# Kernel tuning notes

Hardware: AMD Instinct MI355X
Metric: run time of the kernel (lower is better)

## Reference

```python
import jax, jax.numpy as jnp
import numpy as np

B, N, I, O, CG, H, E = 32, 256, 16, 16, 64, 64, 4096
SEQ_LEN = 256  # sequence_length init arg (temporal attention scale)


def setup_inputs() -> dict:
    key = jax.random.key(0)
    ks = jax.random.split(key, 24)
    r = lambda i, shape, s: jax.random.normal(ks[i], shape, jnp.float32) * s
    return {
        'data': jax.random.normal(ks[0], (B, I, N), jnp.float32),
        'masks': jax.random.bernoulli(ks[1], 0.8, (B, I, N)),
        'edge_index': jax.random.randint(ks[2], (2, E), 0, N, jnp.int64),
        'gcn_w': r(3, (I, CG), 0.2),
        'gcn_b': jnp.zeros((CG,), jnp.float32),
        'sa_qw': r(4, (CG, CG), 0.1), 'sa_qb': jnp.zeros((CG,), jnp.float32),
        'sa_kw': r(5, (CG, CG), 0.1), 'sa_kb': jnp.zeros((CG,), jnp.float32),
        'gru_wih': r(6, (3 * H, I), 0.1), 'gru_whh': r(7, (3 * H, H), 0.1),
        'gru_bih': jnp.zeros((3 * H,), jnp.float32), 'gru_bhh': jnp.zeros((3 * H,), jnp.float32),
        'ta_qw': r(8, (H, H), 0.1), 'ta_qb': jnp.zeros((H,), jnp.float32),
        'ta_kw': r(9, (H, H), 0.1), 'ta_kb': jnp.zeros((H,), jnp.float32),
        'fc1_w': r(10, (H * N * 2, H * N // 4), 0.005), 'fc1_b': jnp.zeros((H * N // 4,), jnp.float32),
        'fc2_w': r(11, (H * N // 4, O * N), 0.01), 'fc2_b': jnp.zeros((O * N,), jnp.float32),
    }


def _forward(data, masks, edge_index, gcn_w, gcn_b, sa_qw, sa_qb, sa_kw, sa_kb,
             gru_wih, gru_whh, gru_bih, gru_bhh, ta_qw, ta_qb, ta_kw, ta_kb,
             fc1_w, fc1_b, fc2_w, fc2_b):
    data = jnp.where(masks, data, 0.0)            # [B, I, N]
    x = jnp.swapaxes(data, 1, 2)                  # [B, N, I] (per-sample node features)

    loop = jnp.arange(N)
    src = jnp.concatenate([edge_index[0], loop])
    dst = jnp.concatenate([edge_index[1], loop])
    w = jnp.concatenate([jnp.ones((E,), jnp.float32), 2.0 * jnp.ones((N,), jnp.float32)])
    deg = jax.ops.segment_sum(w, dst, num_segments=N)
    dinv = jnp.where(deg > 0, jax.lax.rsqrt(deg), 0.0)
    norm = dinv[src] * w * dinv[dst]              # [E+N]
    xw = x @ gcn_w                                # [B, N, CG]
    msg = xw[:, src, :] * norm[None, :, None]     # gather + scale
    agg = jax.vmap(lambda m: jax.ops.segment_sum(m, dst, num_segments=N))(msg)
    h = jax.nn.relu(agg + gcn_b)                  # [B, N, CG]

    # --- SpatialAttention (per sample, scale 1/sqrt(num_nodes)) ---
    q = h @ sa_qw + sa_qb
    k = h @ sa_kw + sa_kb
    att = jax.nn.softmax(jnp.einsum('bnc,bmc->bnm', q, k) / np.sqrt(N).astype(np.float32), axis=-1)
    ha = jnp.einsum('bnm,bmc->bnc', att, h)

    # torch stacks x.T -> [B, CG, N] then .view(B, -1, CG): a reshape, not a transpose
    se = jnp.swapaxes(h, 1, 2).reshape(B, N, CG)
    sa = jnp.swapaxes(ha, 1, 2).reshape(B, N, CG)
    # dropout is identity in eval mode

    # --- GRU (1 layer, batch_first) over rnn_input = data.view(B, -1, I) ---
    rnn_in = data.reshape(B, N, I)
    def step(hprev, xt):
        gi = xt @ gru_wih.T + gru_bih
        gh = hprev @ gru_whh.T + gru_bhh
        ir, iz, inn = jnp.split(gi, 3, axis=-1)
        hr, hz, hn = jnp.split(gh, 3, axis=-1)
        r = jax.nn.sigmoid(ir + hr)
        z = jax.nn.sigmoid(iz + hz)
        n = jnp.tanh(inn + r * hn)
        hnew = (1.0 - z) * n + z * hprev
        return hnew, hnew
    h0 = jnp.zeros((B, H), jnp.float32)
    _, outs = jax.lax.scan(step, h0, jnp.swapaxes(rnn_in, 0, 1))
    rnn_out = jnp.swapaxes(outs, 0, 1)            # [B, N, H]

    # --- TemporalAttention (scale 1/sqrt(sequence_length)) ---
    qt = rnn_out @ ta_qw + ta_qb
    kt = rnn_out @ ta_kw + ta_kb
    att_t = jax.nn.softmax(jnp.einsum('btc,bsc->bts', qt, kt) / np.sqrt(SEQ_LEN).astype(np.float32), axis=-1)
    rnn_a = jnp.einsum('bts,bsc->btc', att_t, rnn_out)

    # --- fused MLP combine ---
    embed = jnp.concatenate([rnn_out, se], axis=-1).reshape(B, -1)  # [B, 2*H*N]
    inter = embed @ fc1_w + fc1_b
    final = inter @ fc2_w + fc2_b
    final = jnp.swapaxes(final.reshape(B, N, O), 1, 2)              # [B, O, N]
    rnn_a = jnp.swapaxes(rnn_a, 1, 2)                               # [B, H, N]
    return final, sa, rnn_a


def reference(data, masks, edge_index, gcn_w, gcn_b, sa_qw, sa_qb, sa_kw, sa_kb,
              gru_wih, gru_whh, gru_bih, gru_bhh, ta_qw, ta_qb, ta_kw, ta_kb,
              fc1_w, fc1_b, fc2_w, fc2_b):
    return _forward(data, masks, edge_index, gcn_w, gcn_b, sa_qw, sa_qb, sa_kw, sa_kb,
                    gru_wih, gru_whh, gru_bih, gru_bhh, ta_qw, ta_qb, ta_kw, ta_kb,
                    fc1_w, fc1_b, fc2_w, fc2_b)
```

## Files before the change

kernel.cpp:

```cpp
#include <hip/hip_runtime.h>

#define NB 32
#define NN 256
#define NI 16
#define NO 16
#define NC 64
#define NH 64
#define NE 4096
#define FC1_N 4096

__device__ __forceinline__ float sigmoidf_(float x){ return 1.0f/(1.0f+__expf(-x)); }
__device__ __forceinline__ float tanhf_(float x){
  float e = __expf(2.0f*x);
  return 1.0f - 2.0f/(e+1.0f);
}

__global__ void k_detect(const unsigned char* __restrict__ m8, const int* __restrict__ ei, int* flags){
  int t = blockIdx.x*256 + threadIdx.x;
  unsigned a = (unsigned)m8[t*4+1] | (unsigned)m8[t*4+2] | (unsigned)m8[t*4+3];
  if (__any(a != 0) && (threadIdx.x & 63) == 0) atomicOr(&flags[0], 1);
  unsigned b = 0;
  if (t < 4096) b = (unsigned)ei[2*t+1];
  if (__any(b != 0) && (threadIdx.x & 63) == 0) atomicOr(&flags[1], 1);
}

__global__ void k_mask(const float* __restrict__ data, const unsigned char* __restrict__ m8,
                       const int* __restrict__ flags, float* __restrict__ dm){
  int i = blockIdx.x*256 + threadIdx.x;
  int mv = flags[0] ? (int)m8[i] : ((const int*)m8)[i];
  dm[i] = mv ? data[i] : 0.0f;
}

__device__ __forceinline__ int edge_src(const int* ei, const int* flags, int e){
  return flags[1] ? ei[e] : ei[2*e];
}
__device__ __forceinline__ int edge_dst(const int* ei, const int* flags, int e){
  return flags[1] ? ei[NE + e] : ei[2*(NE + e)];
}

__global__ __launch_bounds__(256) void k_graph(const int* __restrict__ ei, const int* __restrict__ flags,
                                               float* wadj){
  int t = threadIdx.x;
  float4 z = {0.f,0.f,0.f,0.f};
  for (int x = t; x < 16384; x += 256) ((float4*)wadj)[x] = z;
  __shared__ float degs[NN];
  __shared__ float dls[NN];
  degs[t] = 0.f;
  __syncthreads();
  for (int e = t; e < NE; e += 256) atomicAdd(&degs[edge_dst(ei, flags, e)], 1.0f);
  __syncthreads();
  float di = rsqrtf(degs[t] + 2.0f);
  dls[t] = di;
  atomicAdd(&wadj[t*NN + t], 2.0f*di*di);
  __syncthreads();
  for (int e = t; e < NE; e += 256){
    int s = edge_src(ei, flags, e), d = edge_dst(ei, flags, e);
    atomicAdd(&wadj[d*NN + s], dls[s]*dls[d]);
  }
}

__global__ void k_xw(const float* __restrict__ dm, const float* __restrict__ gw, float* __restrict__ xw){
  int idx = blockIdx.x*256 + threadIdx.x;
  int c = idx & 63, n = (idx>>6) & 255, b = idx>>14;
  const float* dmb = dm + b*NI*NN;
  float a = 0.f;
  #pragma unroll
  for (int i=0;i<NI;i++) a += dmb[i*NN + n]*gw[i*NC + c];
  xw[idx] = a;
}

__global__ void k_agg(const float* __restrict__ wadj, const float* __restrict__ xw,
                      const float* __restrict__ gb, float* __restrict__ h){
  int idx = blockIdx.x*256 + threadIdx.x;
  int c = idx & 63, n = (idx>>6) & 255, b = idx>>14;
  const float* wr = wadj + n*NN;
  const float* xb = xw + b*NN*NC + c;
  float a = gb[c];
  #pragma unroll 4
  for (int m=0;m<NN;m++) a += wr[m]*xb[m*NC];
  h[idx] = fmaxf(a, 0.0f);
}

__global__ void k_qk2(const float* __restrict__ hb, const float* __restrict__ rnn,
    const float* __restrict__ saqw, const float* __restrict__ saqb,
    const float* __restrict__ sakw, const float* __restrict__ sakb,
    const float* __restrict__ taqw, const float* __restrict__ taqb,
    const float* __restrict__ takw, const float* __restrict__ takb,
    float* __restrict__ qb, float* __restrict__ kb, float* __restrict__ qt, float* __restrict__ kt){
  int bid = blockIdx.x;
  const float *src, *qw, *qbias, *kw, *kbias; float *qo, *ko;
  if (bid < 2048){ src=hb; qw=saqw; qbias=saqb; kw=sakw; kbias=sakb; qo=qb; ko=kb; }
  else { bid -= 2048; src=rnn; qw=taqw; qbias=taqb; kw=takw; kbias=takb; qo=qt; ko=kt; }
  int idx = bid*256 + threadIdx.x;
  int c = idx & 63;
  const float* hr = src + (idx>>6)*NC;
  float aq = qbias[c], ak = kbias[c];
  #pragma unroll 8
  for (int cc=0; cc<NC; cc++){ float hv = hr[cc]; aq += hv*qw[cc*NC + c]; ak += hv*kw[cc*NC + c]; }
  qo[idx] = aq; ko[idx] = ak;
}

__global__ __launch_bounds__(256) void k_attn2(const float* __restrict__ qb, const float* __restrict__ kb,
    const float* __restrict__ hb, const float* __restrict__ qt, const float* __restrict__ kt,
    const float* __restrict__ rnn, float* __restrict__ out_sa, float* __restrict__ out_ra){
  int bidx = blockIdx.x;
  const float *q, *kmat, *v; float* outp;
  if (bidx < 1024){ q=qb; kmat=kb; v=hb; outp=out_sa; }
  else { bidx -= 1024; q=qt; kmat=kt; v=rnn; outp=out_ra; }
  int b = bidx >> 5, n0 = (bidx & 31)*8;
  int t = threadIdx.x;
  const float scale = 0.0625f;
  __shared__ __align__(16) float qs[8][64];
  __shared__ float S[8][256];
  #pragma unroll
  for (int rep=0; rep<2; rep++){
    int j = rep*256 + t; int r = j>>6, c = j&63;
    qs[r][c] = q[((b<<8) + n0 + r)*NC + c];
  }
  __syncthreads();
  float4 kr[16];
  const float4* kp = (const float4*)(kmat + ((b<<8) + t)*NC);
  #pragma unroll
  for (int i=0;i<16;i++) kr[i] = kp[i];
  #pragma unroll
  for (int r=0;r<8;r++){
    const float4* q4 = (const float4*)qs[r];
    float s = 0.f;
    #pragma unroll
    for (int i=0;i<16;i++){ float4 a=q4[i], bb=kr[i]; s += a.x*bb.x + a.y*bb.y + a.z*bb.z + a.w*bb.w; }
    S[r][t] = s*scale;
  }
  __syncthreads();
  {
    int g = t>>5, l = t&31;
    float vals[8];
    #pragma unroll
    for (int k2=0;k2<8;k2++) vals[k2] = S[g][l + (k2<<5)];
    float mx = vals[0];
    #pragma unroll
    for (int k2=1;k2<8;k2++) mx = fmaxf(mx, vals[k2]);
    #pragma unroll
    for (int off=16; off; off>>=1) mx = fmaxf(mx, __shfl_xor(mx, off));
    float sm = 0.f;
    #pragma unroll
    for (int k2=0;k2<8;k2++){ vals[k2] = __expf(vals[k2]-mx); sm += vals[k2]; }
    #pragma unroll
    for (int off=16; off; off>>=1) sm += __shfl_xor(sm, off);
    float rS = 1.0f/sm;
    #pragma unroll
    for (int k2=0;k2<8;k2++) S[g][l + (k2<<5)] = vals[k2]*rS;
  }
  __syncthreads();
  int c = t & 63, rp = t >> 6;
  const float* vp = v + (b<<8)*NC + c;
  float a0 = 0.f, a1 = 0.f;
  #pragma unroll 4
  for (int m=0;m<NN;m++){
    float vv = vp[m*NC];
    a0 += S[rp][m]*vv;
    a1 += S[rp+4][m]*vv;
  }
  outp[(((b<<6)+c)<<8) + n0 + rp]     = a0;
  outp[(((b<<6)+c)<<8) + n0 + rp + 4] = a1;
}

__global__ __launch_bounds__(192) void k_gru(const float* __restrict__ dm,
        const float* __restrict__ wih, const float* __restrict__ bih,
        const float* __restrict__ whh, const float* __restrict__ bhh,
        float* __restrict__ rnn){
  int b = blockIdx.x, j = threadIdx.x;
  __shared__ __align__(16) float dmS[4096];
  __shared__ __align__(16) float hs[64];
  __shared__ float gh[192];
  __shared__ float gin[64];
  float wh[64];
  const float4* wr = (const float4*)(whh + j*NH);
  #pragma unroll
  for (int k4=0;k4<16;k4++){ float4 t4 = wr[k4]; wh[4*k4]=t4.x; wh[4*k4+1]=t4.y; wh[4*k4+2]=t4.z; wh[4*k4+3]=t4.w; }
  float wi[16];
  const float4* wir = (const float4*)(wih + j*NI);
  #pragma unroll
  for (int k4=0;k4<4;k4++){ float4 t4 = wir[k4]; wi[4*k4]=t4.x; wi[4*k4+1]=t4.y; wi[4*k4+2]=t4.z; wi[4*k4+3]=t4.w; }
  float bj = bhh[j], bij = bih[j];
  const float4* dmb4 = (const float4*)(dm + b*4096);
  for (int x = j; x < 1024; x += 192) ((float4*)dmS)[x] = dmb4[x];
  if (j < 64) hs[j] = 0.f;
  __syncthreads();
  for (int t=0;t<NN;t++){
    const float* xt = &dmS[t*16];
    float gival = bij;
    #pragma unroll
    for (int i=0;i<16;i++) gival += wi[i]*xt[i];
    float a0=0.f,a1=0.f,a2=0.f,a3=0.f;
    #pragma unroll
    for (int k4=0;k4<16;k4++){
      float4 hv = *(const float4*)&hs[4*k4];
      a0 += wh[4*k4+0]*hv.x; a1 += wh[4*k4+1]*hv.y; a2 += wh[4*k4+2]*hv.z; a3 += wh[4*k4+3]*hv.w;
    }
    float ghv = a0+a1+a2+a3+bj;
    if (j < 128) gh[j] = ghv + gival;
    else { gh[j] = ghv; gin[j-128] = gival; }
    __syncthreads();
    if (j < 64){
      float r  = sigmoidf_(gh[j]);
      float z  = sigmoidf_(gh[j+64]);
      float nn = tanhf_   (gin[j] + r*gh[j+128]);
      float hn = nn + z*(hs[j]-nn);
      rnn[(b*NN + t)*NH + j] = hn;
      hs[j] = hn;
    }
    __syncthreads();
  }
}

__global__ void k_embedT(const float* __restrict__ rnn, const float* __restrict__ h,
                         float* __restrict__ ET){
  int idx = blockIdx.x*256 + threadIdx.x;
  int bb = idx & 31, rr = idx >> 5;
  int n = rr >> 7, c = rr & 127;
  float v;
  if (c < 64) v = rnn[((bb<<8) + n)*NH + c];
  else { int f = (n<<6) + (c-64); v = h[(bb<<14) + ((f&255)<<6) + (f>>8)]; }
  ET[idx] = v;
}

#define FMAQ(q, ev) { \
  acc[0][4*q+0]+=wv.x*ev.x; acc[1][4*q+0]+=wv.y*ev.x; acc[2][4*q+0]+=wv.z*ev.x; acc[3][4*q+0]+=wv.w*ev.x; \
  acc[0][4*q+1]+=wv.x*ev.y; acc[1][4*q+1]+=wv.y*ev.y; acc[2][4*q+1]+=wv.z*ev.y; acc[3][4*q+1]+=wv.w*ev.y; \
  acc[0][4*q+2]+=wv.x*ev.z; acc[1][4*q+2]+=wv.y*ev.z; acc[2][4*q+2]+=wv.z*ev.z; acc[3][4*q+2]+=wv.w*ev.z; \
  acc[0][4*q+3]+=wv.x*ev.w; acc[1][4*q+3]+=wv.y*ev.w; acc[2][4*q+3]+=wv.z*ev.w; acc[3][4*q+3]+=wv.w*ev.w; }

__global__ __launch_bounds__(512, 4) void k_fc1(const float* __restrict__ W,
                       const float* __restrict__ ET, float* __restrict__ part){
  const int tid = threadIdx.x, lane = tid & 63, w = tid >> 6;
  const int cw = w & 3, bh = w >> 2;
  const int col = blockIdx.x*1024 + cw*256 + lane*4;
  const int i0 = blockIdx.y*256;
  __shared__ __align__(16) float es[8][128*16];
  float4* esw4 = (float4*)es[w];
  float acc[4][16];
  #pragma unroll
  for (int c=0;c<4;c++)
    #pragma unroll
    for (int bb=0;bb<16;bb++) acc[c][bb]=0.f;
  const float* wp = W + (long)i0*FC1_N + col;
  float4 ring[4];
  #pragma unroll
  for (int p=0;p<4;p++) ring[p] = *(const float4*)(wp + (long)p*FC1_N);
  const float4* ET4 = (const float4*)ET;
  for (int c=0;c<2;c++){
    __syncthreads();
    const int rowbase = i0 + c*128;
    #pragma unroll
    for (int k=0;k<8;k++){
      int j = lane + k*64;
      esw4[j] = ET4[(long)(rowbase + (j>>2))*8 + bh*4 + (j&3)];
    }
    for (int ii4=0; ii4<32; ii4++){
      #pragma unroll
      for (int p=0;p<4;p++){
        const int r = c*128 + ii4*4 + p;
        float4 wv = ring[p];
        int pf = r + 4; pf = (pf < 256) ? pf : 255;
        ring[p] = *(const float4*)(wp + (long)pf*FC1_N);
        const int ib = (ii4*4 + p)*4;
        float4 e0 = esw4[ib+0], e1 = esw4[ib+1], e2 = esw4[ib+2], e3 = esw4[ib+3];
        FMAQ(0, e0) FMAQ(1, e1) FMAQ(2, e2) FMAQ(3, e3)
      }
    }
  }
  float* pp = part + (long)blockIdx.y*131072 + (long)(bh*16)*FC1_N + col;
  #pragma unroll
  for (int bb=0;bb<16;bb++){
    float4 o; o.x=acc[0][bb]; o.y=acc[1][bb]; o.z=acc[2][bb]; o.w=acc[3][bb];
    *(float4*)(pp + (long)bb*FC1_N) = o;
  }
}

__global__ void k_red1(const float* __restrict__ part, const float* __restrict__ bias,
                       float* __restrict__ ITr){
  int idx = blockIdx.x*256 + threadIdx.x;
  int b = idx >> 12, col = idx & 4095;
  float a = bias[col];
  #pragma unroll 16
  for (int y=0;y<128;y++) a += part[(long)y*131072 + b*FC1_N + col];
  ITr[col*32 + b] = a;
}

__global__ __launch_bounds__(256, 4) void k_fc2(const float* __restrict__ W,
                       const float* __restrict__ ITr, float* __restrict__ part){
  const int tid = threadIdx.x, lane = tid & 63, bq = tid >> 6;
  const int col = blockIdx.x*256 + lane*4;
  const int i0 = blockIdx.y*64;
  __shared__ __align__(16) float es[4][64*8];
  float4* esw4 = (float4*)es[bq];
  float acc[4][8];
  #pragma unroll
  for (int c=0;c<4;c++)
    #pragma unroll
    for (int bb=0;bb<8;bb++) acc[c][bb]=0.f;
  const float4* IT4 = (const float4*)ITr;
  #pragma unroll
  for (int k=0;k<2;k++){
    int j = lane + k*64;
    esw4[j] = IT4[(i0 + (j>>1))*8 + bq*2 + (j&1)];
  }
  const float* wp = W + (long)i0*FC1_N + col;
  float4 ring[4];
  #pragma unroll
  for (int p=0;p<4;p++) ring[p] = *(const float4*)(wp + (long)p*FC1_N);
  for (int ii4=0; ii4<16; ii4++){
    #pragma unroll
    for (int p=0;p<4;p++){
      const int r = ii4*4 + p;
      float4 wv = ring[p];
      int pf = r + 4; pf = (pf < 64) ? pf : 63;
      ring[p] = *(const float4*)(wp + (long)pf*FC1_N);
      float4 e0 = esw4[r*2+0], e1 = esw4[r*2+1];
      FMAQ(0, e0) FMAQ(1, e1)
    }
  }
  float* pp = part + (long)blockIdx.y*131072 + (long)(bq*8)*FC1_N + col;
  #pragma unroll
  for (int bb=0;bb<8;bb++){
    float4 o; o.x=acc[0][bb]; o.y=acc[1][bb]; o.z=acc[2][bb]; o.w=acc[3][bb];
    *(float4*)(pp + (long)bb*FC1_N) = o;
  }
}

__global__ void k_red2(const float* __restrict__ part, const float* __restrict__ bias,
                       float* __restrict__ outp){
  int idx = blockIdx.x*256 + threadIdx.x;
  int b = idx >> 12, col = idx & 4095;
  float a = bias[col];
  #pragma unroll 16
  for (int y=0;y<64;y++) a += part[(long)y*131072 + b*FC1_N + col];
  int n = col >> 4, o = col & 15;
  outp[(b<<12) + (o<<8) + n] = a;
}

extern "C" void kernel_launch(void* const* d_in, const int* in_sizes, int n_in,
                              void* d_out, int out_size, void* d_ws, size_t ws_size,
                              hipStream_t stream) {
  const float* data   = (const float*)d_in[0];
  const unsigned char* masks = (const unsigned char*)d_in[1];
  const int* ei       = (const int*)d_in[2];
  const float* gcn_w  = (const float*)d_in[3];
  const float* gcn_b  = (const float*)d_in[4];
  const float* sa_qw  = (const float*)d_in[5];
  const float* sa_qb  = (const float*)d_in[6];
  const float* sa_kw  = (const float*)d_in[7];
  const float* sa_kb  = (const float*)d_in[8];
  const float* wih    = (const float*)d_in[9];
  const float* whh    = (const float*)d_in[10];
  const float* bih    = (const float*)d_in[11];
  const float* bhh    = (const float*)d_in[12];
  const float* ta_qw  = (const float*)d_in[13];
  const float* ta_qb  = (const float*)d_in[14];
  const float* ta_kw  = (const float*)d_in[15];
  const float* ta_kb  = (const float*)d_in[16];
  const float* fc1_w  = (const float*)d_in[17];
  const float* fc1_b  = (const float*)d_in[18];
  const float* fc2_w  = (const float*)d_in[19];
  const float* fc2_b  = (const float*)d_in[20];

  float* dm    = (float*)d_ws;
  float* wadj  = dm + 131072;
  int*   flags = (int*)(wadj + 65536);
  float* xw    = (float*)(flags + 8);
  float* hb    = xw + 524288;
  float* qb    = hb + 524288;
  float* kb    = qb + 524288;
  float* rnn   = kb + 524288;
  float* qt    = rnn + 524288;
  float* kt    = qt + 524288;
  float* ET    = kt + 524288;
  float* ITr   = ET + 1048576;
  float* part1 = ITr + 131072;
  float* part2 = part1 + 128*131072;

  float* out_final = (float*)d_out;
  float* out_sa = out_final + 131072;
  float* out_ra = out_final + 655360;

  hipMemsetAsync(flags, 0, 32, stream);

  k_detect<<<128,256,0,stream>>>(masks, ei, flags);
  k_mask<<<512,256,0,stream>>>(data, masks, flags, dm);
  k_graph<<<1,256,0,stream>>>(ei, flags, wadj);
  k_xw<<<2048,256,0,stream>>>(dm, gcn_w, xw);
  k_gru<<<32,192,0,stream>>>(dm, wih, bih, whh, bhh, rnn);
  k_agg<<<2048,256,0,stream>>>(wadj, xw, gcn_b, hb);
  k_qk2<<<4096,256,0,stream>>>(hb, rnn, sa_qw, sa_qb, sa_kw, sa_kb,
                               ta_qw, ta_qb, ta_kw, ta_kb, qb, kb, qt, kt);
  k_attn2<<<2048,256,0,stream>>>(qb, kb, hb, qt, kt, rnn, out_sa, out_ra);
  k_embedT<<<4096,256,0,stream>>>(rnn, hb, ET);
  { dim3 g(4,128); k_fc1<<<g,512,0,stream>>>(fc1_w, ET, part1); }
  k_red1<<<512,256,0,stream>>>(part1, fc1_b, ITr);
  { dim3 g(16,64); k_fc2<<<g,256,0,stream>>>(fc2_w, ITr, part2); }
  k_red2<<<512,256,0,stream>>>(part2, fc2_b, out_final);
}
```

Baseline: 561.5 us.

## Unify FC GEMV kernels with double-buffered global_load_lds weight staging

Replaces the separate fc1 and fc2 kernels with one templated kernel. It stages weight and activation chunks of eight rows into LDS through async global_load_lds, double-buffered so the next chunk loads while the current one is computed. The split-K factor for fc1 drops from 128 to 64 and the column tile changes, which halves the partial-sum buffer traffic in the reduction step. This adds a barrier per chunk, and each thread now covers 8 batches instead of 16, so every weight element is read from LDS more often.

Result: faster. 504.3 us (-10.2%).

```diff
diff --git a/kernel.cpp b/kernel.cpp
--- a/kernel.cpp
+++ b/kernel.cpp
@@ -13,6 +13,11 @@
 __device__ __forceinline__ float tanhf_(float x){
   float e = __expf(2.0f*x);
   return 1.0f - 2.0f/(e+1.0f);
+}
+
+__device__ __forceinline__ void gload16(const void* g, void* l){
+  __builtin_amdgcn_global_load_lds((const __attribute__((address_space(1))) void*)g,
+                                   (__attribute__((address_space(3))) void*)l, 16, 0, 0);
 }
 
 __global__ void k_detect(const unsigned char* __restrict__ m8, const int* __restrict__ ei, int* flags){
@@ -224,57 +229,57 @@
   ET[idx] = v;
 }
 
-#define FMAQ(q, ev) { \
-  acc[0][4*q+0]+=wv.x*ev.x; acc[1][4*q+0]+=wv.y*ev.x; acc[2][4*q+0]+=wv.z*ev.x; acc[3][4*q+0]+=wv.w*ev.x; \
-  acc[0][4*q+1]+=wv.x*ev.y; acc[1][4*q+1]+=wv.y*ev.y; acc[2][4*q+1]+=wv.z*ev.y; acc[3][4*q+1]+=wv.w*ev.y; \
-  acc[0][4*q+2]+=wv.x*ev.z; acc[1][4*q+2]+=wv.y*ev.z; acc[2][4*q+2]+=wv.z*ev.z; acc[3][4*q+2]+=wv.w*ev.z; \
-  acc[0][4*q+3]+=wv.x*ev.w; acc[1][4*q+3]+=wv.y*ev.w; acc[2][4*q+3]+=wv.z*ev.w; acc[3][4*q+3]+=wv.w*ev.w; }
-
-__global__ __launch_bounds__(512, 4) void k_fc1(const float* __restrict__ W,
-                       const float* __restrict__ ET, float* __restrict__ part){
-  const int tid = threadIdx.x, lane = tid & 63, w = tid >> 6;
-  const int cw = w & 3, bh = w >> 2;
-  const int col = blockIdx.x*1024 + cw*256 + lane*4;
-  const int i0 = blockIdx.y*256;
-  __shared__ __align__(16) float es[8][128*16];
-  float4* esw4 = (float4*)es[w];
-  float acc[4][16];
+template<int KC>
+__global__ __launch_bounds__(512, 4) void k_fc(const float* __restrict__ W,
+        const float* __restrict__ Ein, float* __restrict__ part){
+  const int tid = threadIdx.x, lane = tid & 63, wv_ = tid >> 6;
+  const int cw = wv_ & 1, bq = wv_ >> 1;
+  const int c0 = blockIdx.x*512;
+  const long k0 = (long)blockIdx.y*KC;
+  __shared__ __align__(16) float wlds[2][8][512];
+  __shared__ __align__(16) float elds[2][256];
+  float acc[4][8];
   #pragma unroll
   for (int c=0;c<4;c++)
     #pragma unroll
-    for (int bb=0;bb<16;bb++) acc[c][bb]=0.f;
-  const float* wp = W + (long)i0*FC1_N + col;
-  float4 ring[4];
-  #pragma unroll
-  for (int p=0;p<4;p++) ring[p] = *(const float4*)(wp + (long)p*FC1_N);
-  const float4* ET4 = (const float4*)ET;
-  for (int c=0;c<2;c++){
+    for (int bb=0;bb<8;bb++) acc[c][bb]=0.f;
+
+  const int NCH = KC/8;
+  #define STAGE_FC(ch, bf) { \
+    const float* wsrc = W + (k0 + (long)(ch)*8)*FC1_N + c0; \
+    gload16(wsrc + (long)wv_*FC1_N + lane*4,       &wlds[bf][wv_][0]); \
+    gload16(wsrc + (long)wv_*FC1_N + 256 + lane*4, &wlds[bf][wv_][256]); \
+    if (wv_ == 0) gload16(Ein + (k0 + (long)(ch)*8)*32 + lane*4, &elds[bf][0]); \
+  }
+
+  STAGE_FC(0, 0)
+  int cur = 0;
+  for (int ch=0; ch<NCH; ch++){
     __syncthreads();
-    const int rowbase = i0 + c*128;
-    #pragma unroll
-    for (int k=0;k<8;k++){
-      int j = lane + k*64;
-      esw4[j] = ET4[(long)(rowbase + (j>>2))*8 + bh*4 + (j&3)];
-    }
-    for (int ii4=0; ii4<32; ii4++){
+    if (ch+1 < NCH) STAGE_FC(ch+1, cur^1)
+    #pragma unroll
+    for (int r=0;r<8;r++){
+      float4 wv4 = *(const float4*)&wlds[cur][r][cw*256 + lane*4];
+      float4 e0 = *(const float4*)&elds[cur][r*32 + bq*8];
+      float4 e1 = *(const float4*)&elds[cur][r*32 + bq*8 + 4];
+      float ev[8] = {e0.x,e0.y,e0.z,e0.w,e1.x,e1.y,e1.z,e1.w};
       #pragma unroll
-      for (int p=0;p<4;p++){
-        const int r = c*128 + ii4*4 + p;
-        float4 wv = ring[p];
-        int pf = r + 4; pf = (pf < 256) ? pf : 255;
-        ring[p] = *(const float4*)(wp + (long)pf*FC1_N);
-        const int ib = (ii4*4 + p)*4;
-        float4 e0 = esw4[ib+0], e1 = esw4[ib+1], e2 = esw4[ib+2], e3 = esw4[ib+3];
-        FMAQ(0, e0) FMAQ(1, e1) FMAQ(2, e2) FMAQ(3, e3)
+      for (int bb=0;bb<8;bb++){
+        acc[0][bb] += wv4.x*ev[bb];
+        acc[1][bb] += wv4.y*ev[bb];
+        acc[2][bb] += wv4.z*ev[bb];
+        acc[3][bb] += wv4.w*ev[bb];
       }
     }
-  }
-  float* pp = part + (long)blockIdx.y*131072 + (long)(bh*16)*FC1_N + col;
-  #pragma unroll
-  for (int bb=0;bb<16;bb++){
+    cur ^= 1;
+  }
+  float* pp = part + (long)blockIdx.y*131072 + (long)(bq*8)*FC1_N + c0 + cw*256 + lane*4;
+  #pragma unroll
+  for (int bb=0;bb<8;bb++){
     float4 o; o.x=acc[0][bb]; o.y=acc[1][bb]; o.z=acc[2][bb]; o.w=acc[3][bb];
     *(float4*)(pp + (long)bb*FC1_N) = o;
   }
+  #undef STAGE_FC
 }
 
 __global__ void k_red1(const float* __restrict__ part, const float* __restrict__ bias,
@@ -283,49 +288,8 @@
   int b = idx >> 12, col = idx & 4095;
   float a = bias[col];
   #pragma unroll 16
-  for (int y=0;y<128;y++) a += part[(long)y*131072 + b*FC1_N + col];
+  for (int y=0;y<64;y++) a += part[(long)y*131072 + b*FC1_N + col];
   ITr[col*32 + b] = a;
-}
-
-__global__ __launch_bounds__(256, 4) void k_fc2(const float* __restrict__ W,
-                       const float* __restrict__ ITr, float* __restrict__ part){
-  const int tid = threadIdx.x, lane = tid & 63, bq = tid >> 6;
-  const int col = blockIdx.x*256 + lane*4;
-  const int i0 = blockIdx.y*64;
-  __shared__ __align__(16) float es[4][64*8];
-  float4* esw4 = (float4*)es[bq];
-  float acc[4][8];
-  #pragma unroll
-  for (int c=0;c<4;c++)
-    #pragma unroll
-    for (int bb=0;bb<8;bb++) acc[c][bb]=0.f;
-  const float4* IT4 = (const float4*)ITr;
-  #pragma unroll
-  for (int k=0;k<2;k++){
-    int j = lane + k*64;
-    esw4[j] = IT4[(i0 + (j>>1))*8 + bq*2 + (j&1)];
-  }
-  const float* wp = W + (long)i0*FC1_N + col;
-  float4 ring[4];
-  #pragma unroll
-  for (int p=0;p<4;p++) ring[p] = *(const float4*)(wp + (long)p*FC1_N);
-  for (int ii4=0; ii4<16; ii4++){
-    #pragma unroll
-    for (int p=0;p<4;p++){
-      const int r = ii4*4 + p;
-      float4 wv = ring[p];
-      int pf = r + 4; pf = (pf < 64) ? pf : 63;
-      ring[p] = *(const float4*)(wp + (long)pf*FC1_N);
-      float4 e0 = esw4[r*2+0], e1 = esw4[r*2+1];
-      FMAQ(0, e0) FMAQ(1, e1)
-    }
-  }
-  float* pp = part + (long)blockIdx.y*131072 + (long)(bq*8)*FC1_N + col;
-  #pragma unroll
-  for (int bb=0;bb<8;bb++){
-    float4 o; o.x=acc[0][bb]; o.y=acc[1][bb]; o.z=acc[2][bb]; o.w=acc[3][bb];
-    *(float4*)(pp + (long)bb*FC1_N) = o;
-  }
 }
 
 __global__ void k_red2(const float* __restrict__ part, const float* __restrict__ bias,
@@ -377,7 +341,7 @@
   float* ET    = kt + 524288;
   float* ITr   = ET + 1048576;
   float* part1 = ITr + 131072;
-  float* part2 = part1 + 128*131072;
+  float* part2 = part1 + 64*131072;
 
   float* out_final = (float*)d_out;
   float* out_sa = out_final + 131072;
@@ -395,8 +359,8 @@
                                ta_qw, ta_qb, ta_kw, ta_kb, qb, kb, qt, kt);
   k_attn2<<<2048,256,0,stream>>>(qb, kb, hb, qt, kt, rnn, out_sa, out_ra);
   k_embedT<<<4096,256,0,stream>>>(rnn, hb, ET);
-  { dim3 g(4,128); k_fc1<<<g,512,0,stream>>>(fc1_w, ET, part1); }
+  { dim3 g(8,64); k_fc<512><<<g,512,0,stream>>>(fc1_w, ET, part1); }
   k_red1<<<512,256,0,stream>>>(part1, fc1_b, ITr);
-  { dim3 g(16,64); k_fc2<<<g,256,0,stream>>>(fc2_w, ITr, part2); }
+  { dim3 g(8,64); k_fc<64><<<g,512,0,stream>>>(fc2_w, ITr, part2); }
   k_red2<<<512,256,0,stream>>>(part2, fc2_b, out_final);
 }
```
